# Kernel optimization log

Hardware: AMD Instinct MI355X
Metric: run time of the kernel (lower is better)

## Reference

```python
import jax, jax.numpy as jnp
import numpy as np

V = 128
L = 128
N = 4096

_ALPHA = "abcdefghijklmnopqrstuvwxyz"
TOKENS = (list("+-*/^()=") + [f"temp_{a}" for a in _ALPHA]
          + [str(d) for d in range(10)] + [f"w{i}" for i in range(84)])
assert len(TOKENS) == V
IDX = {t: i for i, t in enumerate(TOKENS)}
TEMPS = [f"temp_{a}" for a in _ALPHA]


def _build_mask_table() -> np.ndarray:
    """mask_table[p, v] = 0 if token v is illegal after prev-token p, else 1.
    Mirrors RuleFilter.single_filter's rho for every possible prev token."""
    M = np.ones((V, V), dtype=np.float32)

    def ban(prev_tokens, banned_tokens):
        cols = [IDX[t] for t in banned_tokens]
        for p in prev_tokens:
            M[IDX[p], cols] = 0.0

    ban(list("+-*/"), list("+-*/)="))          # prev is binary op
    ban(TEMPS, list("(="))                      # prev is temp_* variable
    ban(["="], list("+-*/=)") + TEMPS)         # prev is '='
    ban(["("], list("()+-*/="))                # prev is '('
    ban([")"], list("()") + TEMPS)             # prev is ')'
    ban(["^"], list("+-*/=)"))                 # prev is '^'
    return M


def setup_inputs() -> dict:
    key = jax.random.key(0)
    logits = jax.random.normal(key, (L, N, V), dtype=jnp.float32)
    mask_table = jnp.asarray(_build_mask_table())  # (V, V) rule lookup
    return {"logits": logits, "mask_table": mask_table}


def reference(logits, mask_table):
    """logits: (L, N, V); mask_table: (V, V). Sequential rule masking:
    logits[i] *= mask_table[argmax(filtered logits[i-1])]."""
    first = logits[0]  # row 0 is never filtered

    def step(carry, cur):
        # carry: previously *filtered* logits row (N, V)
        prev_idx = jnp.argmax(carry, axis=-1)          # (N,)
        new = cur * mask_table[prev_idx]               # gather + multiply
        return new, new

    _, rest = jax.lax.scan(step, first, logits[1:])
    return jnp.concatenate([first[None], rest], axis=0)
```

## Files before the change

kernel.cpp:

```cpp
#include <hip/hip_runtime.h>


constexpr int V = 128;
constexpr int L = 128;
constexpr int N = 4096;

__global__ __launch_bounds__(256) void rule_filter_kernel(
    const float* __restrict__ logits,
    const float* __restrict__ mask_table,
    float* __restrict__ out)
{
    __shared__ unsigned int mbits[V * 4];
    for (int w = threadIdx.x; w < V * 4; w += 256) {
        const int row  = w >> 2;
        const int word = w & 3;
        const float* srcm = mask_table + row * V + word * 32;
        unsigned int bits = 0u;
#pragma unroll
        for (int k = 0; k < 32; ++k)
            bits |= (srcm[k] != 0.0f) ? (1u << k) : 0u;
        mbits[w] = bits;
    }
    __syncthreads();

    const int wave = threadIdx.x >> 6;
    const int lane = threadIdx.x & 63;
    const int n    = (blockIdx.x << 2) + wave;

    const size_t base    = (size_t)n * V + (size_t)(lane * 2);
    const size_t rstride = (size_t)N * V;

    const int mword  = lane >> 4;
    const int mshift = (lane & 15) * 2;

    auto ld = [&](int i) -> float2 {
        return *(const float2*)(logits + (size_t)i * rstride + base);
    };
    auto st = [&](int i, float2 v) {
        *(float2*)(out + (size_t)i * rstride + base) = v;
    };

    auto wave_argmax = [&](float2 f) -> int {
        float bv; int bi;
        if (f.y > f.x) { bv = f.y; bi = lane * 2 + 1; }
        else           { bv = f.x; bi = lane * 2;     }
#pragma unroll
        for (int off = 32; off >= 1; off >>= 1) {
            float ov = __shfl_xor(bv, off);
            int   oi = __shfl_xor(bi, off);
            if (ov > bv || (ov == bv && oi < bi)) { bv = ov; bi = oi; }
        }
        return bi;
    };

    constexpr int D = 4;
    float2 buf[D];
#pragma unroll
    for (int j = 0; j < D; ++j) buf[j] = ld(j);

    st(0, buf[0]);
    int prev = wave_argmax(buf[0]);

#pragma unroll 4
    for (int i = 1; i < L; ++i) {
        float2 c = buf[i & (D - 1)];
        const int pf = (i + D - 1 < L) ? (i + D - 1) : (L - 1);
        buf[pf & (D - 1)] = ld(pf);

        const unsigned int word = mbits[prev * 4 + mword];
        const unsigned int b    = (word >> mshift) & 3u;
        float2 f;
        f.x = (b & 1u) ? c.x : 0.0f;
        f.y = (b & 2u) ? c.y : 0.0f;

        st(i, f);
        prev = wave_argmax(f);
    }
}

extern "C" void kernel_launch(void* const* d_in, const int* in_sizes, int n_in,
                              void* d_out, int out_size, void* d_ws, size_t ws_size,
                              hipStream_t stream) {
    const float* logits     = (const float*)d_in[0];
    const float* mask_table = (const float*)d_in[1];
    float* out              = (float*)d_out;

    dim3 grid(N / 4);
    dim3 block(256);
    rule_filter_kernel<<<grid, block, 0, stream>>>(logits, mask_table, out);
}
```

Before: 513.7 us.

## Use DPP max plus ballot argmax, register mask table, deeper prefetch

Replaces the shuffle-based argmax (value and index shuffles each step) with a DPP row-shift max reduction followed by two ballots and find-first-set, which shortens the serial per-step dependency chain. The shared-memory bitmask table is replaced by per-lane register words holding that lane's mask bits for every previous token, selected with a branchless mux, which drops the LDS lookup and the block barrier. The prefetch depth is raised from 4 to 8 and stores become nontemporal. The cost is more registers per thread, which may reduce occupancy. The DPP row controls also need to produce a correct full-wave max.

```diff
diff --git a/kernel.cpp b/kernel.cpp
--- a/kernel.cpp
+++ b/kernel.cpp
@@ -1,28 +1,55 @@
 #include <hip/hip_runtime.h>
+#include <string.h>
 
 
 constexpr int V = 128;
 constexpr int L = 128;
 constexpr int N = 4096;
 
+__device__ __forceinline__ float wave_max_dpp(float x) {
+    int v = __float_as_int(x);
+    const int ninf = __float_as_int(-__builtin_inff());
+#define RF_STEP(ctrl)                                                          \
+    {                                                                          \
+        int s = __builtin_amdgcn_update_dpp(ninf, v, ctrl, 0xf, 0xf, false);   \
+        v = __float_as_int(fmaxf(__int_as_float(v), __int_as_float(s)));       \
+    }
+    RF_STEP(0x111)
+    RF_STEP(0x112)
+    RF_STEP(0x114)
+    RF_STEP(0x118)
+    RF_STEP(0x142)
+    RF_STEP(0x143)
+#undef RF_STEP
+    return __int_as_float(__builtin_amdgcn_readlane(v, 63));
+}
+
+__device__ __forceinline__ int wave_argmax(float2 f) {
+    const float bv = wave_max_dpp(fmaxf(f.x, f.y));
+    unsigned long long b0 = __ballot(f.x == bv);
+    unsigned long long b1 = __ballot(f.y == bv);
+    int i0 = __ffsll(b0);
+    int i1 = __ffsll(b1);
+    int c0 = i0 ? (i0 - 1) * 2 : (1 << 30);
+    int c1 = i1 ? (i1 - 1) * 2 + 1 : (1 << 30);
+    return min(c0, c1);
+}
+
+__device__ __forceinline__ unsigned sel8(const unsigned* t, int j) {
+    unsigned a0 = (j & 1) ? t[1] : t[0];
+    unsigned a1 = (j & 1) ? t[3] : t[2];
+    unsigned a2 = (j & 1) ? t[5] : t[4];
+    unsigned a3 = (j & 1) ? t[7] : t[6];
+    unsigned b0 = (j & 2) ? a1 : a0;
+    unsigned b1 = (j & 2) ? a3 : a2;
+    return (j & 4) ? b1 : b0;
+}
+
 __global__ __launch_bounds__(256) void rule_filter_kernel(
     const float* __restrict__ logits,
     const float* __restrict__ mask_table,
     float* __restrict__ out)
 {
-    __shared__ unsigned int mbits[V * 4];
-    for (int w = threadIdx.x; w < V * 4; w += 256) {
-        const int row  = w >> 2;
-        const int word = w & 3;
-        const float* srcm = mask_table + row * V + word * 32;
-        unsigned int bits = 0u;
-#pragma unroll
-        for (int k = 0; k < 32; ++k)
-            bits |= (srcm[k] != 0.0f) ? (1u << k) : 0u;
-        mbits[w] = bits;
-    }
-    __syncthreads();
-
     const int wave = threadIdx.x >> 6;
     const int lane = threadIdx.x & 63;
     const int n    = (blockIdx.x << 2) + wave;
@@ -30,48 +57,47 @@
     const size_t base    = (size_t)n * V + (size_t)(lane * 2);
     const size_t rstride = (size_t)N * V;
 
-    const int mword  = lane >> 4;
-    const int mshift = (lane & 15) * 2;
+    unsigned tbl[8];
+#pragma unroll 1
+    for (int j = 0; j < 8; ++j) {
+        unsigned acc = 0;
+#pragma unroll
+        for (int r = 0; r < 16; ++r) {
+            const int p = j * 16 + r;
+            float2 mv = *(const float2*)(mask_table + (size_t)p * V + lane * 2);
+            acc |= ((mv.x != 0.0f ? 1u : 0u) | (mv.y != 0.0f ? 2u : 0u)) << (2 * r);
+        }
+        tbl[j] = acc;
+    }
 
     auto ld = [&](int i) -> float2 {
         return *(const float2*)(logits + (size_t)i * rstride + base);
     };
     auto st = [&](int i, float2 v) {
-        *(float2*)(out + (size_t)i * rstride + base) = v;
+        long long bits;
+        memcpy(&bits, &v, 8);
+        __builtin_nontemporal_store(bits, (long long*)(out + (size_t)i * rstride + base));
     };
 
-    auto wave_argmax = [&](float2 f) -> int {
-        float bv; int bi;
-        if (f.y > f.x) { bv = f.y; bi = lane * 2 + 1; }
-        else           { bv = f.x; bi = lane * 2;     }
-#pragma unroll
-        for (int off = 32; off >= 1; off >>= 1) {
-            float ov = __shfl_xor(bv, off);
-            int   oi = __shfl_xor(bi, off);
-            if (ov > bv || (ov == bv && oi < bi)) { bv = ov; bi = oi; }
-        }
-        return bi;
-    };
-
-    constexpr int D = 4;
+    constexpr int D = 8;
     float2 buf[D];
 #pragma unroll
-    for (int j = 0; j < D; ++j) buf[j] = ld(j);
+    for (int k = 0; k < D; ++k) buf[k] = ld(k);
 
     st(0, buf[0]);
     int prev = wave_argmax(buf[0]);
 
-#pragma unroll 4
+#pragma unroll 8
     for (int i = 1; i < L; ++i) {
         float2 c = buf[i & (D - 1)];
         const int pf = (i + D - 1 < L) ? (i + D - 1) : (L - 1);
         buf[pf & (D - 1)] = ld(pf);
 
-        const unsigned int word = mbits[prev * 4 + mword];
-        const unsigned int b    = (word >> mshift) & 3u;
+        const unsigned word  = sel8(tbl, prev >> 4);
+        const unsigned fbits = (word >> ((prev & 15) * 2)) & 3u;
         float2 f;
-        f.x = (b & 1u) ? c.x : 0.0f;
-        f.y = (b & 2u) ? c.y : 0.0f;
+        f.x = (fbits & 1u) ? c.x : 0.0f;
+        f.y = (fbits & 2u) ? c.y : 0.0f;
 
         st(i, f);
         prev = wave_argmax(f);
```

Measured after the change: 490.3 us. 4.6% less time.
